# Kernel tuning notes

Measured on AMD Instinct MI355X. Metric: run time of the kernel, lower is better.

Reference implementation:

```python
import jax, jax.numpy as jnp
import numpy as np

B, N, D, H = 256, 1000, 128, 8
DH = D // H
CLIP = 10.0  # tanh logit clipping as in Kool et al. / rl4co LogitAttention


def setup_inputs() -> dict:
    key = jax.random.key(0)
    ks = jax.random.split(key, 5)
    w = lambda k, shape: jax.random.normal(k, shape, jnp.float32) * 0.02
    return {
        "embeddings": jax.random.normal(ks[0], (B, N, D), jnp.float32),
        "W_node": w(ks[1], (D, 3 * D)),      # project_node_embeddings (no bias)
        "W_fixed": w(ks[2], (D, D)),          # project_fixed_context (no bias)
        "W_context": w(ks[3], (2 * D, D)),    # TSP context embedding: concat(first, cur) -> d
        "W_out": w(ks[4], (D, D)),            # LogitAttention project_out
        "num_steps": 64,
    }


def reference(embeddings, W_node, W_fixed, W_context, W_out, num_steps):
    # _precompute_cache: fixed glimpse K/V and logit K; dynamic embedding is 0 (TSP StaticEmbedding)
    gk, gv, lk = jnp.split(embeddings @ W_node, 3, axis=-1)     # each [B, N, D]
    graph_ctx = embeddings.mean(1) @ W_fixed                     # [B, D]
    gk_h = gk.reshape(B, N, H, DH)
    gv_h = gv.reshape(B, N, H, DH)

    barange = jnp.arange(B)
    first = jnp.zeros((B,), jnp.int32)                           # start node 0
    visited0 = jnp.zeros((B, N), bool).at[barange, first].set(True)
    first_emb = embeddings[barange, first]                       # [B, D]

    def step(carry, _):
        cur, visited = carry
        cur_emb = embeddings[barange, cur]                       # [B, D]
        # context embedding + graph context -> glimpse query
        ctx = jnp.concatenate([first_emb, cur_emb], axis=-1) @ W_context + graph_ctx
        q = ctx.reshape(B, H, DH)
        # masked multi-head glimpse attention over all nodes
        scores = jnp.einsum("bhd,bnhd->bhn", q, gk_h) / jnp.sqrt(jnp.float32(DH))
        scores = jnp.where(visited[:, None, :], -jnp.inf, scores)
        attn = jax.nn.softmax(scores, axis=-1)
        glimpse = jnp.einsum("bhn,bnhd->bhd", attn, gv_h).reshape(B, D) @ W_out
        # single-head logits with tanh clipping, masked log-softmax
        logits = jnp.einsum("bd,bnd->bn", glimpse, lk) / jnp.sqrt(jnp.float32(D))
        logits = jnp.where(visited, -jnp.inf, CLIP * jnp.tanh(logits))
        log_p = jax.nn.log_softmax(logits, axis=-1)              # [B, N]
        action = jnp.argmax(log_p, axis=-1).astype(jnp.int32)    # greedy decode
        visited = visited.at[barange, action].set(True)
        return (action, visited), (log_p, action)

    _, (log_ps, actions) = jax.lax.scan(step, (first, visited0), None, length=num_steps)
    # outputs [B, steps, N], actions [B, steps]
    return jnp.swapaxes(log_ps, 0, 1), jnp.swapaxes(actions, 0, 1)
```

## Files before the change

### kernel.cpp

```cpp
#include <hip/hip_runtime.h>
#include <math.h>

#define BB 256
#define NN 1000
#define DD 128
#define HH 8
#define NP 1024
#define CHROWS 128
#define CLIPV 10.0f
#define SC_QK 0.25f
#define SC_LG 0.08838834764831845f
#define NEGINF (-INFINITY)
#define LP_FLOOR (-3.0e38f)

typedef float  fx4 __attribute__((ext_vector_type(4)));
typedef unsigned short usx4 __attribute__((ext_vector_type(4)));

__device__ __forceinline__ float dot4(float4 a, float4 b) {
    return fmaf(a.x, b.x, fmaf(a.y, b.y, fmaf(a.z, b.z, a.w * b.w)));
}
__device__ __forceinline__ float4 fma4(float p, float4 e, float4 a) {
    a.x = fmaf(p, e.x, a.x); a.y = fmaf(p, e.y, a.y);
    a.z = fmaf(p, e.z, a.z); a.w = fmaf(p, e.w, a.w);
    return a;
}
__device__ __forceinline__ void bf2f(unsigned int u, float& a, float& b) {
    union { unsigned int i; float f; } lo, hi;
    lo.i = u << 16; hi.i = u & 0xffff0000u;
    a = lo.f; b = hi.f;
}
__device__ __forceinline__ unsigned short f2bf_rne(float x) {
    union { float f; unsigned int u; } v; v.f = x;
    unsigned int r = v.u + 0x7FFFu + ((v.u >> 16) & 1u);
    return (unsigned short)(r >> 16);
}
__device__ __forceinline__ void gl_lds16(const unsigned short* g, unsigned short* l) {
    __builtin_amdgcn_global_load_lds(
        (__attribute__((address_space(1))) void*)(g),
        (__attribute__((address_space(3))) void*)(l), 16, 0, 0);
}

__global__ __launch_bounds__(256) void conv_bf16_pad(const float* __restrict__ emb,
                                                     unsigned short* __restrict__ ebf) {
    const int idx = blockIdx.x * 256 + threadIdx.x;
    const int b   = idx >> 14;
    const int row = (idx >> 4) & 1023;
    const int k8  = idx & 15;
    uint4 o = make_uint4(0u, 0u, 0u, 0u);
    if (row < NN) {
        const float* p = emb + ((size_t)b * NN + row) * DD + k8 * 8;
        fx4 f0 = __builtin_nontemporal_load((const fx4*)p);
        fx4 f1 = __builtin_nontemporal_load((const fx4*)(p + 4));
        o.x = ((unsigned)f2bf_rne(f0.y) << 16) | f2bf_rne(f0.x);
        o.y = ((unsigned)f2bf_rne(f0.w) << 16) | f2bf_rne(f0.z);
        o.z = ((unsigned)f2bf_rne(f1.y) << 16) | f2bf_rne(f1.x);
        o.w = ((unsigned)f2bf_rne(f1.w) << 16) | f2bf_rne(f1.z);
    }
    *(uint4*)(ebf + (size_t)idx * 8) = o;
}

__global__ __launch_bounds__(1024, 4) void ar_decoder_bf16(
    const float* __restrict__ emb,
    const unsigned short* __restrict__ embbf,
    const float* __restrict__ Wn,
    const float* __restrict__ Wf,
    const float* __restrict__ Wc,
    const float* __restrict__ Wo,
    const int*  __restrict__ nsp,
    float* __restrict__ out)
{
    const int b = blockIdx.x;
    const int t = threadIdx.x;
    const int S = nsp[0];
    const float* E  = emb + (size_t)b * (NN * DD);
    const unsigned short* Ebf = embbf + (size_t)b * (1024 * DD);
    const int wv = t >> 6, ln = t & 63;

    __shared__ __align__(16) unsigned short ebuf[3][CHROWS * DD];
    __shared__ __align__(16) float pS[8192];
    __shared__ __align__(16) float qkT[HH * 132];
    __shared__ __align__(16) float wsumL[HH * DD];
    __shared__ __align__(16) float maskF[NP];
    __shared__ __align__(16) float zS[NP];
    __shared__ __align__(16) float ceL[DD], qL[DD], gL[DD], fL[DD], uL[DD];
    __shared__ __align__(16) float fcL[DD], muL[DD], e0L[DD];
    __shared__ __align__(16) float wredM[128], wredS[128];
    __shared__ float mL[HH], lL[HH];
    __shared__ float redA[16], redV[16];
    __shared__ int   redI[16];
    __shared__ float maxvL, logSL;
    __shared__ int   curL, amaxL;

#define STAGE_CHUNK(cidx, bi) do {                                             \
        const unsigned short* _s = Ebf + (size_t)(cidx) * (CHROWS * DD);       \
        unsigned short* _d = &ebuf[bi][0];                                     \
        gl_lds16(_s + wv * 512 + ln * 8,        _d + wv * 512);                \
        gl_lds16(_s + (16 + wv) * 512 + ln * 8, _d + (16 + wv) * 512);         \
    } while (0)
#define SWEEP_STAGE(i, f) do {                                                 \
        if ((i) >= 2 && (i) <= 6) {                                            \
            const int _tc = (f) ? (i) + 1 : 6 - (i);                           \
            STAGE_CHUNK(_tc, _tc % 3);                                         \
        }                                                                      \
    } while (0)

    bool fwd = true;

    STAGE_CHUNK(0, 0);
    STAGE_CHUNK(1, 1);
    STAGE_CHUNK(2, 2);

    {
        const int d = t & 127, strip = t >> 7;
        float acc = 0.f;
        const int n0 = strip * 125;
        for (int k = 0; k < 125; ++k) acc += E[(n0 + k) * DD + d];
        pS[strip * 128 + d] = acc;
    }
    if (t < DD) e0L[t] = E[t];
    __syncthreads();
    if (t < DD) {
        float ssum = 0.f;
        for (int k = 0; k < 8; ++k) ssum += pS[k * 128 + t];
        muL[t] = ssum * (1.0f / (float)NN);
    }
    __syncthreads();
    if (t < DD) {
        float fc = 0.f;
        for (int i = 0; i < DD; ++i)
            fc += muL[i] * Wf[i * DD + t] + e0L[i] * Wc[i * DD + t];
        fcL[t] = fc;
    }
    maskF[t] = (t == 0 || t >= NN) ? NEGINF : 0.f;
    if (t == 0) curL = 0;
    __syncthreads();

    const size_t out_lp_base = (size_t)b * S * NN;
    const size_t act_base    = (size_t)BB * S * NN + (size_t)b * S;

    for (int s = 0; s < S; ++s) {
        if (t < DD) ceL[t] = E[curL * DD + t];
        __syncthreads();
        {
            const int d = t >> 3, p = t & 7;
            const int i0 = p * 16;
            float q = 0.f;
            #pragma unroll
            for (int i = 0; i < 16; ++i)
                q += ceL[i0 + i] * Wc[(DD + i0 + i) * DD + d];
            q += __shfl_xor(q, 1);
            q += __shfl_xor(q, 2);
            q += __shfl_xor(q, 4);
            if (p == 0) qL[d] = q + fcL[d];
        }
        __syncthreads();
        {
            const int h = t >> 7, d = t & 127;
            float v = 0.f;
            for (int k = 0; k < 16; ++k)
                v += Wn[d * 384 + h * 16 + k] * qL[h * 16 + k];
            qkT[h * 132 + d] = v * SC_QK;
        }
        __syncthreads();
        {
            const int dq = t & 3, h = (t >> 2) & 7, o2 = t >> 5;
            float4 qk4[8];
            #pragma unroll
            for (int m = 0; m < 4; ++m) {
                const float* qp = &qkT[h * 132 + (dq + 4 * m) * 8];
                qk4[2 * m]     = *(const float4*)(qp);
                qk4[2 * m + 1] = *(const float4*)(qp + 4);
            }
            float mloc = NEGINF;
            for (int i = 0; i < 8; ++i) {
                const int ck = fwd ? i : 7 - i;
                SWEEP_STAGE(i, fwd);
                const unsigned short* Eb = &ebuf[ck % 3][0];
                float acc[4];
                #pragma unroll
                for (int j = 0; j < 4; ++j) acc[j] = 0.f;
                #pragma unroll
                for (int j = 0; j < 4; ++j) {
                    const int r = o2 * 4 + j;
                    const uint4* rp = (const uint4*)(Eb + r * DD);
                    #pragma unroll
                    for (int m = 0; m < 4; ++m) {
                        uint4 u = rp[dq + 4 * m];
                        float e0,e1,e2,e3,e4,e5,e6,e7;
                        bf2f(u.x, e0, e1); bf2f(u.y, e2, e3);
                        bf2f(u.z, e4, e5); bf2f(u.w, e6, e7);
                        const float4 qa = qk4[2 * m], qb = qk4[2 * m + 1];
                        acc[j] = fmaf(e0, qa.x, fmaf(e1, qa.y, fmaf(e2, qa.z, fmaf(e3, qa.w, acc[j]))));
                        acc[j] = fmaf(e4, qb.x, fmaf(e5, qb.y, fmaf(e6, qb.z, fmaf(e7, qb.w, acc[j]))));
                    }
                }
                #pragma unroll
                for (int j = 0; j < 4; ++j) {
                    acc[j] += __shfl_xor(acc[j], 1);
                    acc[j] += __shfl_xor(acc[j], 2);
                }
                const int nb = ck * 128 + o2 * 4;
                pS[(nb + dq) * 8 + h] = acc[dq];
                #pragma unroll
                for (int j = 0; j < 4; ++j)
                    mloc = fmaxf(mloc, acc[j] + maskF[nb + j]);
                __syncthreads();
            }
            fwd = !fwd;
            mloc = fmaxf(mloc, __shfl_xor(mloc, 1));
            mloc = fmaxf(mloc, __shfl_xor(mloc, 2));
            mloc = fmaxf(mloc, __shfl_xor(mloc, 32));
            if ((t & 35) == 0) wredM[wv * 8 + h] = mloc;
        }
        __syncthreads();
        if (t < HH) {
            float m = wredM[t];
            for (int w = 1; w < 16; ++w) m = fmaxf(m, wredM[w * 8 + t]);
            mL[t] = m;
        }
        __syncthreads();
        {
            float4* pS4 = (float4*)pS;
            float4 a = pS4[t * 2], c = pS4[t * 2 + 1];
            const float mf = maskF[t];
            a.x = expf(a.x + mf - mL[0]); a.y = expf(a.y + mf - mL[1]);
            a.z = expf(a.z + mf - mL[2]); a.w = expf(a.w + mf - mL[3]);
            c.x = expf(c.x + mf - mL[4]); c.y = expf(c.y + mf - mL[5]);
            c.z = expf(c.z + mf - mL[6]); c.w = expf(c.w + mf - mL[7]);
            pS4[t * 2] = a; pS4[t * 2 + 1] = c;
            #pragma unroll
            for (int off = 1; off < 64; off <<= 1) {
                a.x += __shfl_xor(a.x, off); a.y += __shfl_xor(a.y, off);
                a.z += __shfl_xor(a.z, off); a.w += __shfl_xor(a.w, off);
                c.x += __shfl_xor(c.x, off); c.y += __shfl_xor(c.y, off);
                c.z += __shfl_xor(c.z, off); c.w += __shfl_xor(c.w, off);
            }
            if (ln == 0) {
                ((float4*)wredS)[wv * 2] = a;
                ((float4*)wredS)[wv * 2 + 1] = c;
            }
        }
        __syncthreads();
        if (t < HH) {
            float ssum = 0.f;
            for (int w = 0; w < 16; ++w) ssum += wredS[w * 8 + t];
            lL[t] = ssum;
        }
        {
            const int d8 = t & 15, g2 = (t >> 4) & 3, gh = wv & 7, hp = t >> 9;
            float acc[4][8];
            #pragma unroll
            for (int hh = 0; hh < 4; ++hh)
                #pragma unroll
                for (int i = 0; i < 8; ++i) acc[hh][i] = 0.f;
            const float4* pS4 = (const float4*)pS;
            for (int i = 0; i < 8; ++i) {
                const int ck = fwd ? i : 7 - i;
                SWEEP_STAGE(i, fwd);
                const unsigned short* Eb = &ebuf[ck % 3][0];
                #pragma unroll
                for (int k2 = 0; k2 < 4; ++k2) {
                    const int r = k2 * 32 + gh * 4 + g2;
                    const int n = ck * 128 + r;
                    uint4 u = *(const uint4*)(Eb + r * DD + d8 * 8);
                    float e[8];
                    bf2f(u.x, e[0], e[1]); bf2f(u.y, e[2], e[3]);
                    bf2f(u.z, e[4], e[5]); bf2f(u.w, e[6], e[7]);
                    const float4 p4 = pS4[n * 2 + hp];
                    #pragma unroll
                    for (int i2 = 0; i2 < 8; ++i2) {
                        acc[0][i2] = fmaf(p4.x, e[i2], acc[0][i2]);
                        acc[1][i2] = fmaf(p4.y, e[i2], acc[1][i2]);
                        acc[2][i2] = fmaf(p4.z, e[i2], acc[2][i2]);
                        acc[3][i2] = fmaf(p4.w, e[i2], acc[3][i2]);
                    }
                }
                __syncthreads();
            }
            fwd = !fwd;
            #pragma unroll
            for (int hh = 0; hh < 4; ++hh)
                #pragma unroll
                for (int i = 0; i < 8; ++i) {
                    acc[hh][i] += __shfl_xor(acc[hh][i], 16);
                    acc[hh][i] += __shfl_xor(acc[hh][i], 32);
                }
            if (ln < 16) {
                #pragma unroll
                for (int hh = 0; hh < 4; ++hh) {
                    float4* dst = (float4*)&pS[gh * 1024 + (hp * 4 + hh) * 128 + d8 * 8];
                    dst[0] = make_float4(acc[hh][0], acc[hh][1], acc[hh][2], acc[hh][3]);
                    dst[1] = make_float4(acc[hh][4], acc[hh][5], acc[hh][6], acc[hh][7]);
                }
            }
            __syncthreads();
            {
                const int h = t >> 7, d = t & 127;
                float ssum = 0.f;
                #pragma unroll
                for (int g = 0; g < 8; ++g) ssum += pS[g * 1024 + h * 128 + d];
                wsumL[h * DD + d] = ssum;
            }
            __syncthreads();
        }
        {
            const int c = t >> 3, p = t & 7, h = c >> 4;
            const int d0 = p * 16;
            float g = 0.f;
            #pragma unroll
            for (int i = 0; i < 16; ++i)
                g += wsumL[h * DD + d0 + i] * Wn[(d0 + i) * 384 + DD + c];
            g += __shfl_xor(g, 1);
            g += __shfl_xor(g, 2);
            g += __shfl_xor(g, 4);
            if (p == 0) gL[c] = g / lL[h];
        }
        __syncthreads();
        {
            const int d = t >> 3, p = t & 7;
            const int i0 = p * 16;
            float f = 0.f;
            #pragma unroll
            for (int i = 0; i < 16; ++i)
                f += gL[i0 + i] * Wo[(i0 + i) * DD + d];
            f += __shfl_xor(f, 1);
            f += __shfl_xor(f, 2);
            f += __shfl_xor(f, 4);
            if (p == 0) fL[d] = f;
        }
        __syncthreads();
        {
            const int d = t >> 3, p = t & 7;
            const int k0 = p * 16;
            float u = 0.f;
            #pragma unroll
            for (int k = 0; k < 16; ++k)
                u += Wn[d * 384 + 256 + k0 + k] * fL[k0 + k];
            u += __shfl_xor(u, 1);
            u += __shfl_xor(u, 2);
            u += __shfl_xor(u, 4);
            if (p == 0) uL[d] = u * SC_LG;
        }
        __syncthreads();
        {
            const int q8 = t & 7, rr = t >> 3;
            const float4* uL4 = (const float4*)uL;
            const float4 ua0 = uL4[q8 * 2],       ub0 = uL4[q8 * 2 + 1];
            const float4 ua1 = uL4[(q8 + 8) * 2], ub1 = uL4[(q8 + 8) * 2 + 1];
            for (int i = 0; i < 8; ++i) {
                const int ck = fwd ? i : 7 - i;
                SWEEP_STAGE(i, fwd);
                const unsigned short* Eb = &ebuf[ck % 3][0];
                const int n = ck * 128 + rr;
                uint4 u0 = *(const uint4*)(Eb + rr * DD + q8 * 8);
                uint4 u1 = *(const uint4*)(Eb + rr * DD + (q8 + 8) * 8);
                float e0,e1,e2,e3,e4,e5,e6,e7;
                bf2f(u0.x, e0, e1); bf2f(u0.y, e2, e3);
                bf2f(u0.z, e4, e5); bf2f(u0.w, e6, e7);
                float lg;
                lg = fmaf(e0, ua0.x, fmaf(e1, ua0.y, fmaf(e2, ua0.z, e3 * ua0.w)));
                lg = fmaf(e4, ub0.x, fmaf(e5, ub0.y, fmaf(e6, ub0.z, fmaf(e7, ub0.w, lg))));
                bf2f(u1.x, e0, e1); bf2f(u1.y, e2, e3);
                bf2f(u1.z, e4, e5); bf2f(u1.w, e6, e7);
                lg = fmaf(e0, ua1.x, fmaf(e1, ua1.y, fmaf(e2, ua1.z, fmaf(e3, ua1.w, lg))));
                lg = fmaf(e4, ub1.x, fmaf(e5, ub1.y, fmaf(e6, ub1.z, fmaf(e7, ub1.w, lg))));
                lg += __shfl_xor(lg, 1);
                lg += __shfl_xor(lg, 2);
                lg += __shfl_xor(lg, 4);
                if (q8 == 0)
                    zS[n] = (n < NN) ? (CLIPV * tanhf(lg) + maskF[n]) : NEGINF;
                __syncthreads();
            }
            fwd = !fwd;
        }
        {
            const float z = zS[t];
            float v = z; int idx = t;
            #pragma unroll
            for (int off = 1; off < 64; off <<= 1) {
                float v2 = __shfl_xor(v, off);
                int   i2 = __shfl_xor(idx, off);
                if (v2 > v || (v2 == v && i2 < idx)) { v = v2; idx = i2; }
            }
            if (ln == 0) { redV[wv] = v; redI[wv] = idx; }
            __syncthreads();
            if (t == 0) {
                float bv = redV[0]; int bi = redI[0];
                for (int ww = 1; ww < 16; ++ww)
                    if (redV[ww] > bv || (redV[ww] == bv && redI[ww] < bi)) { bv = redV[ww]; bi = redI[ww]; }
                maxvL = bv; amaxL = bi;
            }
            __syncthreads();
            float e = expf(z - maxvL);
            #pragma unroll
            for (int off = 1; off < 64; off <<= 1) e += __shfl_xor(e, off);
            if (ln == 0) redA[wv] = e;
            __syncthreads();
            if (t == 0) {
                float ssum = 0.f;
                for (int ww = 0; ww < 16; ++ww) ssum += redA[ww];
                logSL = logf(ssum);
            }
            __syncthreads();
            if (t < NN) {
                float lp = fmaxf(z - maxvL - logSL, LP_FLOOR);
                __builtin_nontemporal_store(lp, &out[out_lp_base + (size_t)s * NN + t]);
            }
            if (t == 0) {
                __builtin_nontemporal_store((float)amaxL, &out[act_base + s]);
                maskF[amaxL] = NEGINF;
                curL = amaxL;
            }
        }
        __syncthreads();
    }
#undef SWEEP_STAGE
#undef STAGE_CHUNK
}

__global__ __launch_bounds__(1024) void ar_decoder_f32(
    const float* __restrict__ emb, const float* __restrict__ Wn,
    const float* __restrict__ Wf, const float* __restrict__ Wc,
    const float* __restrict__ Wo, const int* __restrict__ nsp,
    float* __restrict__ out)
{
    const int b = blockIdx.x;
    const int t = threadIdx.x;
    const int S = nsp[0];
    const float*  E  = emb + (size_t)b * (NN * DD);
    const float4* E4 = (const float4*)E;

    __shared__ __align__(16) float pS[8192];
    __shared__ __align__(16) float qkT[1024];
    __shared__ __align__(16) float wsumL[HH * DD];
    __shared__ __align__(16) float maskF[NP];
    __shared__ __align__(16) float ceL[DD], qL[DD], gL[DD], fL[DD], uL[DD], fcL[DD], muL[DD], e0L[DD];
    __shared__ float mL[HH], lL[HH];
    __shared__ float redA[16], redV[16];
    __shared__ int   redI[16];
    __shared__ float maxvL, logSL;
    __shared__ int   curL, amaxL;

    {
        const int d = t & 127, strip = t >> 7;
        float acc = 0.f;
        const int n0 = strip * 125;
        for (int k = 0; k < 125; ++k) acc += E[(n0 + k) * DD + d];
        pS[strip * 128 + d] = acc;
    }
    if (t < DD) e0L[t] = E[t];
    __syncthreads();
    if (t < DD) {
        float ssum = 0.f;
        for (int k = 0; k < 8; ++k) ssum += pS[k * 128 + t];
        muL[t] = ssum * (1.0f / (float)NN);
    }
    __syncthreads();
    if (t < DD) {
        float fc = 0.f;
        for (int i = 0; i < DD; ++i)
            fc += muL[i] * Wf[i * DD + t] + e0L[i] * Wc[i * DD + t];
        fcL[t] = fc;
    }
    maskF[t] = (t == 0 || t >= NN) ? NEGINF : 0.f;
    if (t == 0) curL = 0;
    __syncthreads();

    const size_t out_lp_base = (size_t)b * S * NN;
    const size_t act_base    = (size_t)BB * S * NN + (size_t)b * S;

    for (int s = 0; s < S; ++s) {
        if (t < DD) ceL[t] = E[curL * DD + t];
        __syncthreads();
        if (t < DD) {
            float q = fcL[t];
            for (int i = 0; i < DD; ++i) q += ceL[i] * Wc[(DD + i) * DD + t];
            qL[t] = q;
        }
        __syncthreads();
        {
            const int h = t >> 7, d = t & 127;
            float v = 0.f;
            for (int k = 0; k < 16; ++k) v += Wn[d * 384 + h * 16 + k] * qL[h * 16 + k];
            qkT[(d >> 2) * 32 + h * 4 + (d & 3)] = v * SC_QK;
        }
        __syncthreads();
        {
            const int dq = t & 3, h = (t >> 2) & 7, o = t >> 5;
            float4 qk4[8];
            const float4* qkT4 = (const float4*)qkT;
            #pragma unroll
            for (int i = 0; i < 8; ++i) qk4[i] = qkT4[(i * 4 + dq) * 8 + h];
            for (int oi = 0; oi < 4; ++oi) {
                const int oe = oi * 32 + o;
                float acc[8] = {0,0,0,0,0,0,0,0};
                #pragma unroll
                for (int i = 0; i < 8; ++i) {
                    const int d4 = i * 4 + dq;
                    #pragma unroll
                    for (int j = 0; j < 8; ++j) {
                        int row = oe * 8 + j; if (row > NN - 1) row = NN - 1;
                        acc[j] += dot4(E4[row * 32 + d4], qk4[i]);
                    }
                }
                #pragma unroll
                for (int j = 0; j < 8; ++j) {
                    acc[j] += __shfl_xor(acc[j], 1);
                    acc[j] += __shfl_xor(acc[j], 2);
                }
                const int j0 = 2 * dq;
                pS[(oe * 8 + j0)     * 8 + h] = acc[j0];
                pS[(oe * 8 + j0 + 1) * 8 + h] = acc[j0 + 1];
            }
        }
        __syncthreads();
        {
            const int w = t >> 6, lane = t & 63;
            const int h = w & 7, half = (w >> 3) * 512;
            float m = NEGINF;
            for (int k = 0; k < 8; ++k) {
                const int n = half + k * 64 + lane;
                m = fmaxf(m, pS[n * 8 + h] + maskF[n]);
            }
            for (int off = 32; off > 0; off >>= 1) m = fmaxf(m, __shfl_xor(m, off));
            if (lane == 0) redA[w] = m;
        }
        __syncthreads();
        if (t < HH) mL[t] = fmaxf(redA[t], redA[8 + t]);
        __syncthreads();
        {
            float4* pS4 = (float4*)pS;
            float4 a = pS4[t * 2], c = pS4[t * 2 + 1];
            const float mf = maskF[t];
            a.x = expf(a.x + mf - mL[0]); a.y = expf(a.y + mf - mL[1]);
            a.z = expf(a.z + mf - mL[2]); a.w = expf(a.w + mf - mL[3]);
            c.x = expf(c.x + mf - mL[4]); c.y = expf(c.y + mf - mL[5]);
            c.z = expf(c.z + mf - mL[6]); c.w = expf(c.w + mf - mL[7]);
            pS4[t * 2] = a; pS4[t * 2 + 1] = c;
        }
        __syncthreads();
        {
            const int w = t >> 6, lane = t & 63;
            const int h = w & 7, half = (w >> 3) * 512;
            float sum = 0.f;
            for (int k = 0; k < 8; ++k) sum += pS[(half + k * 64 + lane) * 8 + h];
            for (int off = 32; off > 0; off >>= 1) sum += __shfl_xor(sum, off);
            if (lane == 0) redA[w] = sum;
        }
        __syncthreads();
        if (t < HH) lL[t] = redA[t] + redA[8 + t];
        __syncthreads();
        {
            float4 acc[8];
            const int d4 = t & 31, nq = t >> 5;
            #pragma unroll
            for (int h = 0; h < 8; ++h) acc[h] = make_float4(0, 0, 0, 0);
            const float4* pS4 = (const float4*)pS;
            for (int k = 0; k < 32; ++k) {
                const int n = nq * 32 + k;
                const int row = (n > NN - 1) ? NN - 1 : n;
                float4 e4 = E4[row * 32 + d4];
                float4 pa = pS4[n * 2], pb = pS4[n * 2 + 1];
                acc[0] = fma4(pa.x, e4, acc[0]); acc[1] = fma4(pa.y, e4, acc[1]);
                acc[2] = fma4(pa.z, e4, acc[2]); acc[3] = fma4(pa.w, e4, acc[3]);
                acc[4] = fma4(pb.x, e4, acc[4]); acc[5] = fma4(pb.y, e4, acc[5]);
                acc[6] = fma4(pb.z, e4, acc[6]); acc[7] = fma4(pb.w, e4, acc[7]);
            }
            __syncthreads();
            #pragma unroll
            for (int h = 0; h < 8; ++h) {
                acc[h].x += __shfl_xor(acc[h].x, 32);
                acc[h].y += __shfl_xor(acc[h].y, 32);
                acc[h].z += __shfl_xor(acc[h].z, 32);
                acc[h].w += __shfl_xor(acc[h].w, 32);
            }
            const int w = t >> 6, lane = t & 63;
            float4* red4 = (float4*)pS;
            for (int rh = 0; rh < 2; ++rh) {
                if (lane < 32) {
                    #pragma unroll
                    for (int hh = 0; hh < 4; ++hh)
                        red4[(w * 4 + hh) * 32 + d4] = acc[rh * 4 + hh];
                }
                __syncthreads();
                if (t < 512) {
                    const int hh = t >> 7, d = t & 127;
                    float ssum = 0.f;
                    for (int ww = 0; ww < 16; ++ww) ssum += pS[(ww * 4 + hh) * 128 + d];
                    wsumL[(rh * 4 + hh) * DD + d] = ssum;
                }
                __syncthreads();
            }
        }
        if (t < DD) {
            const int h = t >> 4;
            float g = 0.f;
            for (int d = 0; d < DD; ++d) g += wsumL[h * DD + d] * Wn[d * 384 + DD + t];
            gL[t] = g / lL[h];
        }
        __syncthreads();
        if (t < DD) {
            float f = 0.f;
            for (int i = 0; i < DD; ++i) f += gL[i] * Wo[i * DD + t];
            fL[t] = f;
        }
        __syncthreads();
        if (t < DD) {
            float u = 0.f;
            for (int k = 0; k < DD; ++k) u += Wn[t * 384 + 256 + k] * fL[k];
            uL[t] = u * SC_LG;
        }
        __syncthreads();
        {
            const int row = (t > NN - 1) ? NN - 1 : t;
            float lg = 0.f;
            const float4* uL4 = (const float4*)uL;
            for (int d4 = 0; d4 < 32; ++d4) lg += dot4(E4[row * 32 + d4], uL4[d4]);
            const float z = CLIPV * tanhf(lg) + maskF[t];
            float v = z; int idx = t;
            for (int off = 1; off < 64; off <<= 1) {
                float v2 = __shfl_xor(v, off);
                int   i2 = __shfl_xor(idx, off);
                if (v2 > v || (v2 == v && i2 < idx)) { v = v2; idx = i2; }
            }
            const int w = t >> 6, lane = t & 63;
            if (lane == 0) { redV[w] = v; redI[w] = idx; }
            __syncthreads();
            if (t == 0) {
                float bv = redV[0]; int bi = redI[0];
                for (int ww = 1; ww < 16; ++ww)
                    if (redV[ww] > bv || (redV[ww] == bv && redI[ww] < bi)) { bv = redV[ww]; bi = redI[ww]; }
                maxvL = bv; amaxL = bi;
            }
            __syncthreads();
            float e = expf(z - maxvL);
            for (int off = 1; off < 64; off <<= 1) e += __shfl_xor(e, off);
            if (lane == 0) redA[w] = e;
            __syncthreads();
            if (t == 0) {
                float ssum = 0.f;
                for (int ww = 0; ww < 16; ++ww) ssum += redA[ww];
                logSL = logf(ssum);
            }
            __syncthreads();
            if (t < NN) {
                float lp = z - maxvL - logSL;
                out[out_lp_base + (size_t)s * NN + t] = fmaxf(lp, LP_FLOOR);
            }
            if (t == 0) {
                out[act_base + s] = (float)amaxL;
                maskF[amaxL] = NEGINF;
                curL = amaxL;
            }
        }
        __syncthreads();
    }
}

extern "C" void kernel_launch(void* const* d_in, const int* in_sizes, int n_in,
                              void* d_out, int out_size, void* d_ws, size_t ws_size,
                              hipStream_t stream) {
    const float* emb = (const float*)d_in[0];
    const float* Wn  = (const float*)d_in[1];
    const float* Wf  = (const float*)d_in[2];
    const float* Wc  = (const float*)d_in[3];
    const float* Wo  = (const float*)d_in[4];
    const int*   nsp = (const int*)d_in[5];
    const size_t need = (size_t)BB * 1024 * DD * sizeof(unsigned short);
    if (ws_size >= need) {
        unsigned short* ebf = (unsigned short*)d_ws;
        const int nunits = BB * 1024 * 16;
        conv_bf16_pad<<<dim3(nunits / 256), dim3(256), 0, stream>>>(emb, ebf);
        ar_decoder_bf16<<<dim3(BB), dim3(1024), 0, stream>>>(emb, ebf, Wn, Wf, Wc, Wo, nsp, (float*)d_out);
    } else {
        ar_decoder_f32<<<dim3(BB), dim3(1024), 0, stream>>>(emb, Wn, Wf, Wc, Wo, nsp, (float*)d_out);
    }
}
```

Before: 4.693 ms.

## Fuse glimpse score and value passes using Cauchy-Schwarz softmax bound

Replaces the two-pass glimpse attention (scores, then max, exp, sum, then a second sweep for the weighted value sum) with a single sweep over the embedding chunks. The softmax shift is taken from an upper bound, the norm of the per-head query times the maximum embedding row norm computed once at kernel start, rather than from the true maximum. The exponentials and the P·V accumulation then happen per chunk. This removes one full pass over the staged bf16 embeddings and several reductions and barriers per step. The cost is an extra barrier per chunk and a risk of exp underflow if the bound is much larger than the true maximum.

```diff
diff --git a/kernel.cpp b/kernel.cpp
--- a/kernel.cpp
+++ b/kernel.cpp
@@ -84,8 +84,10 @@
     __shared__ __align__(16) float zS[NP];
     __shared__ __align__(16) float ceL[DD], qL[DD], gL[DD], fL[DD], uL[DD];
     __shared__ __align__(16) float fcL[DD], muL[DD], e0L[DD];
-    __shared__ __align__(16) float wredM[128], wredS[128];
-    __shared__ float mL[HH], lL[HH];
+    __shared__ __align__(16) float wredS[128];
+    __shared__ float mM[HH];
+    __shared__ float lL[HH];
+    __shared__ float enormL;
     __shared__ float redA[16], redV[16];
     __shared__ int   redI[16];
     __shared__ float maxvL, logSL;
@@ -134,6 +136,29 @@
     maskF[t] = (t == 0 || t >= NN) ? NEGINF : 0.f;
     if (t == 0) curL = 0;
     __syncthreads();
+    {
+        const float4* E4 = (const float4*)E;
+        const int j = t & 31, rq = t >> 5;
+        float mx = 0.f;
+        for (int it = 0; it < 32; ++it) {
+            const int r = it * 32 + rq;
+            float s2 = 0.f;
+            if (r < NN) { float4 v = E4[r * 32 + j]; s2 = dot4(v, v); }
+            s2 += __shfl_xor(s2, 1);  s2 += __shfl_xor(s2, 2);
+            s2 += __shfl_xor(s2, 4);  s2 += __shfl_xor(s2, 8);
+            s2 += __shfl_xor(s2, 16);
+            mx = fmaxf(mx, s2);
+        }
+        mx = fmaxf(mx, __shfl_xor(mx, 32));
+        if (ln == 0) redA[wv] = mx;
+        __syncthreads();
+        if (t == 0) {
+            float m = redA[0];
+            for (int w = 1; w < 16; ++w) m = fmaxf(m, redA[w]);
+            enormL = sqrtf(m) * 1.01f + 1e-3f;
+        }
+        __syncthreads();
+    }
 
     const size_t out_lp_base = (size_t)b * S * NN;
     const size_t act_base    = (size_t)BB * S * NN + (size_t)b * S;
@@ -159,11 +184,20 @@
             float v = 0.f;
             for (int k = 0; k < 16; ++k)
                 v += Wn[d * 384 + h * 16 + k] * qL[h * 16 + k];
-            qkT[h * 132 + d] = v * SC_QK;
-        }
+            v *= SC_QK;
+            qkT[h * 132 + d] = v;
+            float q2 = v * v;
+            q2 += __shfl_xor(q2, 1);  q2 += __shfl_xor(q2, 2);
+            q2 += __shfl_xor(q2, 4);  q2 += __shfl_xor(q2, 8);
+            q2 += __shfl_xor(q2, 16); q2 += __shfl_xor(q2, 32);
+            if (ln == 0) redA[wv] = q2;
+        }
+        __syncthreads();
+        if (t < HH) mM[t] = sqrtf(redA[2 * t] + redA[2 * t + 1]) * enormL + 1e-6f;
         __syncthreads();
         {
             const int dq = t & 3, h = (t >> 2) & 7, o2 = t >> 5;
+            const int d8 = t & 15, g2 = (t >> 4) & 3, gh = wv & 7, hp = t >> 9;
             float4 qk4[8];
             #pragma unroll
             for (int m = 0; m < 4; ++m) {
@@ -171,7 +205,13 @@
                 qk4[2 * m]     = *(const float4*)(qp);
                 qk4[2 * m + 1] = *(const float4*)(qp + 4);
             }
-            float mloc = NEGINF;
+            const float Mh = mM[h];
+            float accw[4][8];
+            #pragma unroll
+            for (int hh = 0; hh < 4; ++hh)
+                #pragma unroll
+                for (int e8 = 0; e8 < 8; ++e8) accw[hh][e8] = 0.f;
+            float lacc = 0.f;
             for (int i = 0; i < 8; ++i) {
                 const int ck = fwd ? i : 7 - i;
                 SWEEP_STAGE(i, fwd);
@@ -200,106 +240,64 @@
                     acc[j] += __shfl_xor(acc[j], 2);
                 }
                 const int nb = ck * 128 + o2 * 4;
-                pS[(nb + dq) * 8 + h] = acc[dq];
-                #pragma unroll
-                for (int j = 0; j < 4; ++j)
-                    mloc = fmaxf(mloc, acc[j] + maskF[nb + j]);
+                const float pt = expf(acc[dq] + maskF[nb + dq] - Mh);
+                pS[(o2 * 4 + dq) * 8 + h] = pt;
+                lacc += pt;
                 __syncthreads();
+                {
+                    const float4* pSc4 = (const float4*)pS;
+                    #pragma unroll
+                    for (int k2 = 0; k2 < 4; ++k2) {
+                        const int r = k2 * 32 + gh * 4 + g2;
+                        uint4 u = *(const uint4*)(Eb + r * DD + d8 * 8);
+                        float e[8];
+                        bf2f(u.x, e[0], e[1]); bf2f(u.y, e[2], e[3]);
+                        bf2f(u.z, e[4], e[5]); bf2f(u.w, e[6], e[7]);
+                        const float4 p4 = pSc4[r * 2 + hp];
+                        #pragma unroll
+                        for (int e8 = 0; e8 < 8; ++e8) {
+                            accw[0][e8] = fmaf(p4.x, e[e8], accw[0][e8]);
+                            accw[1][e8] = fmaf(p4.y, e[e8], accw[1][e8]);
+                            accw[2][e8] = fmaf(p4.z, e[e8], accw[2][e8]);
+                            accw[3][e8] = fmaf(p4.w, e[e8], accw[3][e8]);
+                        }
+                    }
+                }
+                __syncthreads();
             }
             fwd = !fwd;
-            mloc = fmaxf(mloc, __shfl_xor(mloc, 1));
-            mloc = fmaxf(mloc, __shfl_xor(mloc, 2));
-            mloc = fmaxf(mloc, __shfl_xor(mloc, 32));
-            if ((t & 35) == 0) wredM[wv * 8 + h] = mloc;
-        }
-        __syncthreads();
-        if (t < HH) {
-            float m = wredM[t];
-            for (int w = 1; w < 16; ++w) m = fmaxf(m, wredM[w * 8 + t]);
-            mL[t] = m;
-        }
-        __syncthreads();
-        {
-            float4* pS4 = (float4*)pS;
-            float4 a = pS4[t * 2], c = pS4[t * 2 + 1];
-            const float mf = maskF[t];
-            a.x = expf(a.x + mf - mL[0]); a.y = expf(a.y + mf - mL[1]);
-            a.z = expf(a.z + mf - mL[2]); a.w = expf(a.w + mf - mL[3]);
-            c.x = expf(c.x + mf - mL[4]); c.y = expf(c.y + mf - mL[5]);
-            c.z = expf(c.z + mf - mL[6]); c.w = expf(c.w + mf - mL[7]);
-            pS4[t * 2] = a; pS4[t * 2 + 1] = c;
-            #pragma unroll
-            for (int off = 1; off < 64; off <<= 1) {
-                a.x += __shfl_xor(a.x, off); a.y += __shfl_xor(a.y, off);
-                a.z += __shfl_xor(a.z, off); a.w += __shfl_xor(a.w, off);
-                c.x += __shfl_xor(c.x, off); c.y += __shfl_xor(c.y, off);
-                c.z += __shfl_xor(c.z, off); c.w += __shfl_xor(c.w, off);
-            }
-            if (ln == 0) {
-                ((float4*)wredS)[wv * 2] = a;
-                ((float4*)wredS)[wv * 2 + 1] = c;
-            }
-        }
-        __syncthreads();
-        if (t < HH) {
-            float ssum = 0.f;
-            for (int w = 0; w < 16; ++w) ssum += wredS[w * 8 + t];
-            lL[t] = ssum;
-        }
-        {
-            const int d8 = t & 15, g2 = (t >> 4) & 3, gh = wv & 7, hp = t >> 9;
-            float acc[4][8];
+            lacc += __shfl_xor(lacc, 1);
+            lacc += __shfl_xor(lacc, 2);
+            lacc += __shfl_xor(lacc, 32);
+            if ((ln & 35) == 0) wredS[wv * 8 + h] = lacc;
             #pragma unroll
             for (int hh = 0; hh < 4; ++hh)
                 #pragma unroll
-                for (int i = 0; i < 8; ++i) acc[hh][i] = 0.f;
-            const float4* pS4 = (const float4*)pS;
-            for (int i = 0; i < 8; ++i) {
-                const int ck = fwd ? i : 7 - i;
-                SWEEP_STAGE(i, fwd);
-                const unsigned short* Eb = &ebuf[ck % 3][0];
-                #pragma unroll
-                for (int k2 = 0; k2 < 4; ++k2) {
-                    const int r = k2 * 32 + gh * 4 + g2;
-                    const int n = ck * 128 + r;
-                    uint4 u = *(const uint4*)(Eb + r * DD + d8 * 8);
-                    float e[8];
-                    bf2f(u.x, e[0], e[1]); bf2f(u.y, e[2], e[3]);
-                    bf2f(u.z, e[4], e[5]); bf2f(u.w, e[6], e[7]);
-                    const float4 p4 = pS4[n * 2 + hp];
-                    #pragma unroll
-                    for (int i2 = 0; i2 < 8; ++i2) {
-                        acc[0][i2] = fmaf(p4.x, e[i2], acc[0][i2]);
-                        acc[1][i2] = fmaf(p4.y, e[i2], acc[1][i2]);
-                        acc[2][i2] = fmaf(p4.z, e[i2], acc[2][i2]);
-                        acc[3][i2] = fmaf(p4.w, e[i2], acc[3][i2]);
-                    }
-                }
-                __syncthreads();
-            }
-            fwd = !fwd;
-            #pragma unroll
-            for (int hh = 0; hh < 4; ++hh)
-                #pragma unroll
-                for (int i = 0; i < 8; ++i) {
-                    acc[hh][i] += __shfl_xor(acc[hh][i], 16);
-                    acc[hh][i] += __shfl_xor(acc[hh][i], 32);
-                }
+                for (int e8 = 0; e8 < 8; ++e8) {
+                    accw[hh][e8] += __shfl_xor(accw[hh][e8], 16);
+                    accw[hh][e8] += __shfl_xor(accw[hh][e8], 32);
+                }
+            __syncthreads();
             if (ln < 16) {
                 #pragma unroll
                 for (int hh = 0; hh < 4; ++hh) {
                     float4* dst = (float4*)&pS[gh * 1024 + (hp * 4 + hh) * 128 + d8 * 8];
-                    dst[0] = make_float4(acc[hh][0], acc[hh][1], acc[hh][2], acc[hh][3]);
-                    dst[1] = make_float4(acc[hh][4], acc[hh][5], acc[hh][6], acc[hh][7]);
+                    dst[0] = make_float4(accw[hh][0], accw[hh][1], accw[hh][2], accw[hh][3]);
+                    dst[1] = make_float4(accw[hh][4], accw[hh][5], accw[hh][6], accw[hh][7]);
                 }
             }
             __syncthreads();
             {
-                const int h = t >> 7, d = t & 127;
+                const int h2 = t >> 7, d = t & 127;
                 float ssum = 0.f;
                 #pragma unroll
-                for (int g = 0; g < 8; ++g) ssum += pS[g * 1024 + h * 128 + d];
-                wsumL[h * DD + d] = ssum;
+                for (int g = 0; g < 8; ++g) ssum += pS[g * 1024 + h2 * 128 + d];
+                wsumL[h2 * DD + d] = ssum;
+            }
+            if (t < HH) {
+                float ssum = 0.f;
+                for (int w = 0; w < 16; ++w) ssum += wredS[w * 8 + t];
+                lL[t] = ssum;
             }
             __syncthreads();
         }
```

Measured after the change: 9.801 ms. 109% more time.
